# Kernel tuning notes

Measured on AMD Instinct MI355X. Metric: run time of the kernel, lower is better.

## Reference

```python
import jax, jax.numpy as jnp
import numpy as np

VOCAB = 32000
EMB = 256
HID = 512
SEQ = 512
SOS = 1  # word2vec key_to_index['<SOS>']; PAD assumed index 0 and never sampled


def setup_inputs() -> dict:
    key = jax.random.key(0)
    ks = jax.random.split(key, 8)
    k_lstm = 1.0 / np.sqrt(HID)
    k_out = 1.0 / np.sqrt(HID)
    return {
        # token ids in [2, VOCAB) so the PAD-skip branch never triggers
        "input_seq": jax.random.randint(ks[0], (1, SEQ), 2, VOCAB, dtype=jnp.int32),
        "h0": jnp.zeros((1, 1, HID), jnp.float32),
        "c0": jnp.zeros((1, 1, HID), jnp.float32),
        "embedding": jax.random.normal(ks[1], (VOCAB, EMB), jnp.float32) * 0.02,
        "W_ih": jax.random.uniform(ks[2], (4 * HID, EMB), jnp.float32, -k_lstm, k_lstm),
        "W_hh": jax.random.uniform(ks[3], (4 * HID, HID), jnp.float32, -k_lstm, k_lstm),
        "b_ih": jax.random.uniform(ks[4], (4 * HID,), jnp.float32, -k_lstm, k_lstm),
        "b_hh": jax.random.uniform(ks[5], (4 * HID,), jnp.float32, -k_lstm, k_lstm),
        "W_out": jax.random.uniform(ks[6], (VOCAB, HID), jnp.float32, -k_out, k_out),
        "b_out": jax.random.uniform(ks[7], (VOCAB,), jnp.float32, -k_out, k_out),
    }


def reference(input_seq, h0, c0, embedding, W_ih, W_hh, b_ih, b_hh, W_out, b_out):
    # tokens actually fed to the LSTM: <SOS> then the full teacher-forced sequence
    tokens = jnp.concatenate([jnp.array([SOS], jnp.int32), input_seq[0]])  # [S+1]
    emb = embedding[tokens]  # [S+1, E]
    bias = b_ih + b_hh

    def cell(carry, x_t):
        h, c = carry  # [H], [H]
        gates = W_ih @ x_t + W_hh @ h + bias  # [4H], torch gate order i,f,g,o
        i, f, g, o = jnp.split(gates, 4)
        i = jax.nn.sigmoid(i)
        f = jax.nn.sigmoid(f)
        g = jnp.tanh(g)
        o = jax.nn.sigmoid(o)
        c_new = f * c + i * g
        h_new = o * jnp.tanh(c_new)
        return (h_new, c_new), h_new

    (hT, cT), hs = jax.lax.scan(cell, (h0[0, 0], c0[0, 0]), emb)  # hs: [S+1, H]
    logits = hs @ W_out.T + b_out  # [S+1, V] (same math as per-step Linear + cat)
    outputs = logits[None]  # [1, S+1, V]
    return outputs, hT[None, None], cT[None, None]
```

## Files before the change

kernel.cpp:

```cpp
#include <hip/hip_runtime.h>
#include <cmath>

#define VOCAB 32000
#define EMB   256
#define HID   512
#define TLEN  513
#define G4    2048
#define NWG   32
#define SOS   1

typedef unsigned long long u64;
typedef unsigned int uivec4 __attribute__((ext_vector_type(4)));
typedef float f32x4 __attribute__((ext_vector_type(4)));
typedef short bf16x8 __attribute__((ext_vector_type(8)));

__device__ inline float fsig(float x)  { return __builtin_amdgcn_rcpf(1.f + __expf(-x)); }
__device__ inline float ftanh(float x) { return 1.f - 2.f * __builtin_amdgcn_rcpf(__expf(2.f * x) + 1.f); }

__device__ inline void bf16split(float f, short& h, short& l) {
    unsigned u = __float_as_uint(f);
    unsigned r = u + (0x7fffu + ((u >> 16) & 1u));
    unsigned hb = r & 0xffff0000u;
    h = (short)(hb >> 16);
    float res = f - __uint_as_float(hb);
    unsigned u2 = __float_as_uint(res);
    unsigned r2 = u2 + (0x7fffu + ((u2 >> 16) & 1u));
    l = (short)(r2 >> 16);
}

__global__ __launch_bounds__(256) void precompute_gates(
    const int* __restrict__ seq, const float* __restrict__ emb,
    const float* __restrict__ W_ih, const float* __restrict__ b_ih,
    const float* __restrict__ b_hh, float* __restrict__ Xg)
{
    __shared__ __align__(16) float ebuf[16][EMB];
    const int bt = blockIdx.x;
    const int br = blockIdx.y;
    const int tid = threadIdx.x;

    for (int tt = 0; tt < 16; ++tt) {
        int t = bt * 16 + tt;
        if (t < TLEN) {
            int tok = (t == 0) ? SOS : seq[t - 1];
            ebuf[tt][tid] = emb[(size_t)tok * EMB + tid];
        }
    }
    __syncthreads();

    const int row = br * 256 + tid;
    float acc[16];
#pragma unroll
    for (int tt = 0; tt < 16; ++tt) acc[tt] = 0.f;

    const float4* wp = (const float4*)(W_ih + (size_t)row * EMB);
#pragma unroll 4
    for (int k4 = 0; k4 < EMB / 4; ++k4) {
        float4 w = wp[k4];
#pragma unroll
        for (int tt = 0; tt < 16; ++tt) {
            float4 e = *(const float4*)&ebuf[tt][k4 * 4];
            acc[tt] = fmaf(w.x, e.x, fmaf(w.y, e.y, fmaf(w.z, e.z, fmaf(w.w, e.w, acc[tt]))));
        }
    }

    const float bias = b_ih[row] + b_hh[row];
    for (int tt = 0; tt < 16; ++tt) {
        int t = bt * 16 + tt;
        if (t < TLEN) Xg[(size_t)t * G4 + row] = acc[tt] + bias;
    }
}

__global__ __launch_bounds__(256, 1) void lstm_recurrence(
    const float* __restrict__ Xg, const float* __restrict__ W_hh,
    const float* __restrict__ h0, const float* __restrict__ c0,
    float* __restrict__ hs, u64* pk,
    float* __restrict__ out_hT, float* __restrict__ out_cT)
{
    __shared__ __align__(16) float hbuf[HID];
    __shared__ float pbuf[256];

    const int wg  = blockIdx.x;
    const int tid = threadIdx.x;
    const int wv  = tid >> 6;
    const int ln  = tid & 63;
    const int q   = ln >> 4;
    const int j   = ln & 15;
    const int row = q * HID + wg * 16 + j;

    float4 wreg[32];
    const float4* wp = (const float4*)(W_hh + (size_t)row * HID + wv * 128);
#pragma unroll
    for (int i = 0; i < 32; ++i) wreg[i] = wp[i];

    float c = (tid < 16) ? c0[wg * 16 + tid] : 0.f;
    {
        float2 h2 = *(const float2*)&h0[tid * 2];
        hbuf[tid * 2]     = h2.x;
        hbuf[tid * 2 + 1] = h2.y;
    }
    __syncthreads();

    for (int t = 0; t < TLEN; ++t) {
        float xg0 = 0.f, xg1 = 0.f, xg2 = 0.f, xg3 = 0.f;
        if (tid < 16) {
            const float* xp = Xg + (size_t)t * G4 + wg * 16 + tid;
            xg0 = xp[0]; xg1 = xp[512]; xg2 = xp[1024]; xg3 = xp[1536];
        }

        if (t > 0) {
            const unsigned tt = (unsigned)t;
            u64 sa = (u64)(uintptr_t)(pk + (size_t)(t & 1) * HID + 2 * tid);
            asm volatile("s_waitcnt vmcnt(0)" ::: "memory");
            uivec4 rA, rB;
            asm volatile("global_load_dwordx4 %0, %1, off sc0 sc1"
                         : "=v"(rA) : "v"(sa));
            asm volatile("global_load_dwordx4 %0, %1, off sc0 sc1\n\t"
                         "s_waitcnt vmcnt(1)"
                         : "=v"(rB) : "v"(sa));
            unsigned w0, w1;
            for (;;) {
                if (rA.y == tt && rA.w == tt) { w0 = rA.x; w1 = rA.z; break; }
                asm volatile("global_load_dwordx4 %0, %1, off sc0 sc1\n\t"
                             "s_waitcnt vmcnt(1)"
                             : "=v"(rA) : "v"(sa));
                if (rB.y == tt && rB.w == tt) { w0 = rB.x; w1 = rB.z; break; }
                asm volatile("global_load_dwordx4 %0, %1, off sc0 sc1\n\t"
                             "s_waitcnt vmcnt(1)"
                             : "=v"(rB) : "v"(sa));
            }
            asm volatile("s_waitcnt vmcnt(0)" : : "v"(rA), "v"(rB));
            hbuf[2 * tid]     = __uint_as_float(w0);
            hbuf[2 * tid + 1] = __uint_as_float(w1);
            __syncthreads();
        }

        float acc8[8];
#pragma unroll
        for (int i = 0; i < 8; ++i) acc8[i] = 0.f;
#pragma unroll
        for (int i = 0; i < 32; ++i) {
            float4 w4 = wreg[i];
            float4 h4 = *(const float4*)&hbuf[wv * 128 + i * 4];
            acc8[i & 7] = fmaf(w4.x, h4.x, fmaf(w4.y, h4.y,
                          fmaf(w4.z, h4.z, fmaf(w4.w, h4.w, acc8[i & 7]))));
        }
        pbuf[tid] = ((acc8[0] + acc8[1]) + (acc8[2] + acc8[3]))
                  + ((acc8[4] + acc8[5]) + (acc8[6] + acc8[7]));
        __syncthreads();

        if (tid < 16) {
            float gi = pbuf[tid]      + pbuf[64 + tid]  + pbuf[128 + tid] + pbuf[192 + tid] + xg0;
            float gf = pbuf[16 + tid] + pbuf[80 + tid]  + pbuf[144 + tid] + pbuf[208 + tid] + xg1;
            float gg = pbuf[32 + tid] + pbuf[96 + tid]  + pbuf[160 + tid] + pbuf[224 + tid] + xg2;
            float go = pbuf[48 + tid] + pbuf[112 + tid] + pbuf[176 + tid] + pbuf[240 + tid] + xg3;
            float i_ = fsig(gi);
            float f_ = fsig(gf);
            float g_ = ftanh(gg);
            float o_ = fsig(go);
            c = fmaf(f_, c, i_ * g_);
            float h_ = o_ * ftanh(c);
            if (t < TLEN - 1) {
                u64 word = ((u64)(unsigned)(t + 1) << 32) | (u64)__float_as_uint(h_);
                __hip_atomic_store(&pk[(size_t)((t + 1) & 1) * HID + wg * 16 + tid], word,
                                   __ATOMIC_RELAXED, __HIP_MEMORY_SCOPE_AGENT);
            } else {
                out_hT[wg * 16 + tid] = h_;
                out_cT[wg * 16 + tid] = c;
            }
            hs[(size_t)t * HID + wg * 16 + tid] = h_;
        }
    }
}

#define GLDT 40

__global__ __launch_bounds__(256, 2) void out_gemm_mfma(
    const float* __restrict__ hs, const float* __restrict__ W_out,
    const float* __restrict__ b_out, float* __restrict__ out)
{
    __shared__ __align__(16) short Ah[128][GLDT];
    __shared__ __align__(16) short Al[128][GLDT];
    __shared__ __align__(16) short Bh[128][GLDT];
    __shared__ __align__(16) short Bl[128][GLDT];

    const int tb = blockIdx.x;
    const int vb = blockIdx.y;
    const int tid = threadIdx.x;
    const int w   = tid >> 6;
    const int l   = tid & 63;
    const int l15 = l & 15;
    const int lg  = l >> 4;
    const int m0 = tb * 128, n0 = vb * 128;

    const int sr = tid >> 1;
    const int kh = (tid & 1) * 16;

    f32x4 acc[2][8];
#pragma unroll
    for (int s = 0; s < 2; ++s)
#pragma unroll
        for (int cc = 0; cc < 8; ++cc) acc[s][cc] = (f32x4){0.f, 0.f, 0.f, 0.f};

    for (int k0 = 0; k0 < HID; k0 += 32) {
        {
            int trow = m0 + sr;
            float4 fa0 = make_float4(0.f,0.f,0.f,0.f), fa1 = fa0, fa2 = fa0, fa3 = fa0;
            if (trow < TLEN) {
                const float4* ap = (const float4*)(hs + (size_t)trow * HID + k0 + kh);
                fa0 = ap[0]; fa1 = ap[1]; fa2 = ap[2]; fa3 = ap[3];
            }
            float fv[16] = { fa0.x,fa0.y,fa0.z,fa0.w, fa1.x,fa1.y,fa1.z,fa1.w,
                             fa2.x,fa2.y,fa2.z,fa2.w, fa3.x,fa3.y,fa3.z,fa3.w };
#pragma unroll
            for (int g = 0; g < 2; ++g) {
                union { short s[8]; bf16x8 v; } ph, pl;
#pragma unroll
                for (int e = 0; e < 8; ++e) bf16split(fv[g * 8 + e], ph.s[e], pl.s[e]);
                *(bf16x8*)&Ah[sr][kh + 8 * g] = ph.v;
                *(bf16x8*)&Al[sr][kh + 8 * g] = pl.v;
            }
        }
        {
            const float4* bp = (const float4*)(W_out + (size_t)(n0 + sr) * HID + k0 + kh);
            float4 fb0 = bp[0], fb1 = bp[1], fb2 = bp[2], fb3 = bp[3];
            float fv[16] = { fb0.x,fb0.y,fb0.z,fb0.w, fb1.x,fb1.y,fb1.z,fb1.w,
                             fb2.x,fb2.y,fb2.z,fb2.w, fb3.x,fb3.y,fb3.z,fb3.w };
#pragma unroll
            for (int g = 0; g < 2; ++g) {
                union { short s[8]; bf16x8 v; } ph, pl;
#pragma unroll
                for (int e = 0; e < 8; ++e) bf16split(fv[g * 8 + e], ph.s[e], pl.s[e]);
                *(bf16x8*)&Bh[sr][kh + 8 * g] = ph.v;
                *(bf16x8*)&Bl[sr][kh + 8 * g] = pl.v;
            }
        }
        __syncthreads();

        bf16x8 ah[2], al2[2];
#pragma unroll
        for (int s = 0; s < 2; ++s) {
            ah[s]  = *(const bf16x8*)&Ah[32 * w + 16 * s + l15][8 * lg];
            al2[s] = *(const bf16x8*)&Al[32 * w + 16 * s + l15][8 * lg];
        }
#pragma unroll
        for (int cc = 0; cc < 8; ++cc) {
            bf16x8 bh = *(const bf16x8*)&Bh[16 * cc + l15][8 * lg];
            bf16x8 bl = *(const bf16x8*)&Bl[16 * cc + l15][8 * lg];
#pragma unroll
            for (int s = 0; s < 2; ++s) {
                acc[s][cc] = __builtin_amdgcn_mfma_f32_16x16x32_bf16(ah[s],  bh, acc[s][cc], 0, 0, 0);
                acc[s][cc] = __builtin_amdgcn_mfma_f32_16x16x32_bf16(ah[s],  bl, acc[s][cc], 0, 0, 0);
                acc[s][cc] = __builtin_amdgcn_mfma_f32_16x16x32_bf16(al2[s], bh, acc[s][cc], 0, 0, 0);
            }
        }
        __syncthreads();
    }

#pragma unroll
    for (int cc = 0; cc < 8; ++cc) {
        int col = n0 + 16 * cc + l15;
        float bo = b_out[col];
#pragma unroll
        for (int s = 0; s < 2; ++s) {
            int rbase = m0 + 32 * w + 16 * s + lg * 4;
#pragma unroll
            for (int r = 0; r < 4; ++r) {
                int trow = rbase + r;
                if (trow < TLEN) out[(size_t)trow * VOCAB + col] = acc[s][cc][r] + bo;
            }
        }
    }
}

extern "C" void kernel_launch(void* const* d_in, const int* in_sizes, int n_in,
                              void* d_out, int out_size, void* d_ws, size_t ws_size,
                              hipStream_t stream)
{
    const int*   seq   = (const int*)  d_in[0];
    const float* h0    = (const float*)d_in[1];
    const float* c0    = (const float*)d_in[2];
    const float* emb   = (const float*)d_in[3];
    const float* W_ih  = (const float*)d_in[4];
    const float* W_hh  = (const float*)d_in[5];
    const float* b_ih  = (const float*)d_in[6];
    const float* b_hh  = (const float*)d_in[7];
    const float* W_out = (const float*)d_in[8];
    const float* b_out = (const float*)d_in[9];

    float* out_logits = (float*)d_out;
    float* out_hT     = out_logits + (size_t)TLEN * VOCAB;
    float* out_cT     = out_hT + HID;

    float* Xg = (float*)d_ws;
    float* hs = Xg + (size_t)TLEN * G4;
    u64*   pk = (u64*)(hs + (size_t)TLEN * HID);

    hipMemsetAsync(pk, 0, 2 * HID * sizeof(u64), stream);
    precompute_gates<<<dim3(33, 8), 256, 0, stream>>>(seq, emb, W_ih, b_ih, b_hh, Xg);
    lstm_recurrence<<<NWG, 256, 0, stream>>>(Xg, W_hh, h0, c0, hs, pk, out_hT, out_cT);
    out_gemm_mfma<<<dim3(5, 250), 256, 0, stream>>>(hs, W_out, b_out, out_logits);
}
```

Before: 1.073 ms.

## Add L2-local fast-path flag exchange with XCD-aware block placement in LSTM recurrence

The recurrence grid is launched with 249 blocks and only every eighth block does work. On a GPU that deals blocks round-robin across XCDs, this would put all 32 working blocks on the same XCD. Each step's h is published both to a system-coherent buffer and to a second buffer written and polled with sc0 only, so the poll can hit the shared L2 instead of going further out. The fast path has a bounded spin count and falls back to the coherent poll if any lane times out. The pbuf partial-sum buffer is double-buffered so the barrier after writing hbuf can be dropped. This relies on undocumented block-to-XCD placement, and the removed barrier may introduce races.

```diff
diff --git a/kernel.cpp b/kernel.cpp
--- a/kernel.cpp
+++ b/kernel.cpp
@@ -73,13 +73,15 @@
 __global__ __launch_bounds__(256, 1) void lstm_recurrence(
     const float* __restrict__ Xg, const float* __restrict__ W_hh,
     const float* __restrict__ h0, const float* __restrict__ c0,
-    float* __restrict__ hs, u64* pk,
+    float* __restrict__ hs, u64* pk, u64* pf,
     float* __restrict__ out_hT, float* __restrict__ out_cT)
 {
     __shared__ __align__(16) float hbuf[HID];
-    __shared__ float pbuf[256];
-
-    const int wg  = blockIdx.x;
+    __shared__ float pbuf[2][256];
+
+    const int bx = blockIdx.x;
+    if (bx & 7) return;
+    const int wg  = bx >> 3;
     const int tid = threadIdx.x;
     const int wv  = tid >> 6;
     const int ln  = tid & 63;
@@ -100,6 +102,8 @@
     }
     __syncthreads();
 
+    bool usefast = true;
+
     for (int t = 0; t < TLEN; ++t) {
         float xg0 = 0.f, xg1 = 0.f, xg2 = 0.f, xg3 = 0.f;
         if (tid < 16) {
@@ -109,29 +113,29 @@
 
         if (t > 0) {
             const unsigned tt = (unsigned)t;
-            u64 sa = (u64)(uintptr_t)(pk + (size_t)(t & 1) * HID + 2 * tid);
-            asm volatile("s_waitcnt vmcnt(0)" ::: "memory");
-            uivec4 rA, rB;
-            asm volatile("global_load_dwordx4 %0, %1, off sc0 sc1"
-                         : "=v"(rA) : "v"(sa));
-            asm volatile("global_load_dwordx4 %0, %1, off sc0 sc1\n\t"
-                         "s_waitcnt vmcnt(1)"
-                         : "=v"(rB) : "v"(sa));
-            unsigned w0, w1;
-            for (;;) {
-                if (rA.y == tt && rA.w == tt) { w0 = rA.x; w1 = rA.z; break; }
-                asm volatile("global_load_dwordx4 %0, %1, off sc0 sc1\n\t"
-                             "s_waitcnt vmcnt(1)"
-                             : "=v"(rA) : "v"(sa));
-                if (rB.y == tt && rB.w == tt) { w0 = rB.x; w1 = rB.z; break; }
-                asm volatile("global_load_dwordx4 %0, %1, off sc0 sc1\n\t"
-                             "s_waitcnt vmcnt(1)"
-                             : "=v"(rB) : "v"(sa));
-            }
-            asm volatile("s_waitcnt vmcnt(0)" : : "v"(rA), "v"(rB));
-            hbuf[2 * tid]     = __uint_as_float(w0);
-            hbuf[2 * tid + 1] = __uint_as_float(w1);
-            __syncthreads();
+            const size_t off = (size_t)(t & 1) * HID + 2 * tid;
+            uivec4 r;
+            bool got = false;
+            if (usefast) {
+                u64 fa = (u64)(uintptr_t)(pf + off);
+                const int K = (t == 1) ? 128 : 64;
+                for (int it = 0; it < K; ++it) {
+                    asm volatile("global_load_dwordx4 %0, %1, off sc0\n\t"
+                                 "s_waitcnt vmcnt(0)" : "=v"(r) : "v"(fa));
+                    if (r.y == tt && r.w == tt) { got = true; break; }
+                }
+                if (__ballot(got ? 1 : 0) != ~0ull) usefast = false;
+            }
+            if (!got) {
+                u64 sa = (u64)(uintptr_t)(pk + off);
+                do {
+                    asm volatile("global_load_dwordx4 %0, %1, off sc0 sc1\n\t"
+                                 "s_waitcnt vmcnt(0)" : "=v"(r) : "v"(sa));
+                } while (r.y != tt || r.w != tt);
+            }
+            hbuf[2 * tid]     = __uint_as_float(r.x);
+            hbuf[2 * tid + 1] = __uint_as_float(r.z);
+            asm volatile("s_waitcnt lgkmcnt(0)" ::: "memory");
         }
 
         float acc8[8];
@@ -144,15 +148,16 @@
             acc8[i & 7] = fmaf(w4.x, h4.x, fmaf(w4.y, h4.y,
                           fmaf(w4.z, h4.z, fmaf(w4.w, h4.w, acc8[i & 7]))));
         }
-        pbuf[tid] = ((acc8[0] + acc8[1]) + (acc8[2] + acc8[3]))
-                  + ((acc8[4] + acc8[5]) + (acc8[6] + acc8[7]));
+        pbuf[t & 1][tid] = ((acc8[0] + acc8[1]) + (acc8[2] + acc8[3]))
+                         + ((acc8[4] + acc8[5]) + (acc8[6] + acc8[7]));
         __syncthreads();
 
         if (tid < 16) {
-            float gi = pbuf[tid]      + pbuf[64 + tid]  + pbuf[128 + tid] + pbuf[192 + tid] + xg0;
-            float gf = pbuf[16 + tid] + pbuf[80 + tid]  + pbuf[144 + tid] + pbuf[208 + tid] + xg1;
-            float gg = pbuf[32 + tid] + pbuf[96 + tid]  + pbuf[160 + tid] + pbuf[224 + tid] + xg2;
-            float go = pbuf[48 + tid] + pbuf[112 + tid] + pbuf[176 + tid] + pbuf[240 + tid] + xg3;
+            const float* pb = pbuf[t & 1];
+            float gi = pb[tid]      + pb[64 + tid]  + pb[128 + tid] + pb[192 + tid] + xg0;
+            float gf = pb[16 + tid] + pb[80 + tid]  + pb[144 + tid] + pb[208 + tid] + xg1;
+            float gg = pb[32 + tid] + pb[96 + tid]  + pb[160 + tid] + pb[224 + tid] + xg2;
+            float go = pb[48 + tid] + pb[112 + tid] + pb[176 + tid] + pb[240 + tid] + xg3;
             float i_ = fsig(gi);
             float f_ = fsig(gf);
             float g_ = ftanh(gg);
@@ -161,8 +166,11 @@
             float h_ = o_ * ftanh(c);
             if (t < TLEN - 1) {
                 u64 word = ((u64)(unsigned)(t + 1) << 32) | (u64)__float_as_uint(h_);
-                __hip_atomic_store(&pk[(size_t)((t + 1) & 1) * HID + wg * 16 + tid], word,
-                                   __ATOMIC_RELAXED, __HIP_MEMORY_SCOPE_AGENT);
+                size_t po = (size_t)((t + 1) & 1) * HID + wg * 16 + tid;
+                u64 faddr = (u64)(uintptr_t)(pf + po);
+                asm volatile("global_store_dwordx2 %0, %1, off sc0"
+                             :: "v"(faddr), "v"(word) : "memory");
+                __hip_atomic_store(&pk[po], word, __ATOMIC_RELAXED, __HIP_MEMORY_SCOPE_AGENT);
             } else {
                 out_hT[wg * 16 + tid] = h_;
                 out_cT[wg * 16 + tid] = c;
@@ -294,9 +302,10 @@
     float* Xg = (float*)d_ws;
     float* hs = Xg + (size_t)TLEN * G4;
     u64*   pk = (u64*)(hs + (size_t)TLEN * HID);
-
-    hipMemsetAsync(pk, 0, 2 * HID * sizeof(u64), stream);
+    u64*   pf = pk + 2 * HID;
+
+    hipMemsetAsync(pk, 0, 4 * HID * sizeof(u64), stream);
     precompute_gates<<<dim3(33, 8), 256, 0, stream>>>(seq, emb, W_ih, b_ih, b_hh, Xg);
-    lstm_recurrence<<<NWG, 256, 0, stream>>>(Xg, W_hh, h0, c0, hs, pk, out_hT, out_cT);
+    lstm_recurrence<<<249, 256, 0, stream>>>(Xg, W_hh, h0, c0, hs, pk, pf, out_hT, out_cT);
     out_gemm_mfma<<<dim3(5, 250), 256, 0, stream>>>(hs, W_out, b_out, out_logits);
 }
```

Result: faster. 924.8 us (-13.8%).

## Restructure LSTM recurrence into 128 single-wave blocks with shuffle reductions

Applied to the files above, without the earlier changes.

The recurrence kernel moves from 32 workgroups of 256 threads to 128 single-wavefront blocks, each owning 4 hidden units. W_hh slices stay in registers, the previous h is read straight from the packed flag buffer into registers, and gate reductions use cross-lane shuffles instead of LDS and __syncthreads. The point is to remove intra-block barriers and LDS round trips from the serial per-step critical path. The cost is that 128 blocks now poll the global flag buffer each step. The separate memset of the flag buffer is also folded into the precompute kernel.

```diff
diff --git a/kernel.cpp b/kernel.cpp
--- a/kernel.cpp
+++ b/kernel.cpp
@@ -6,7 +6,7 @@
 #define HID   512
 #define TLEN  513
 #define G4    2048
-#define NWG   32
+#define NWAVE 128
 #define SOS   1
 
 typedef unsigned long long u64;
@@ -16,6 +16,9 @@
 
 __device__ inline float fsig(float x)  { return __builtin_amdgcn_rcpf(1.f + __expf(-x)); }
 __device__ inline float ftanh(float x) { return 1.f - 2.f * __builtin_amdgcn_rcpf(__expf(2.f * x) + 1.f); }
+__device__ inline float fma4(f32x4 w, f32x4 h, float a) {
+    return fmaf(w[0], h[0], fmaf(w[1], h[1], fmaf(w[2], h[2], fmaf(w[3], h[3], a))));
+}
 
 __device__ inline void bf16split(float f, short& h, short& l) {
     unsigned u = __float_as_uint(f);
@@ -31,13 +34,17 @@
 __global__ __launch_bounds__(256) void precompute_gates(
     const int* __restrict__ seq, const float* __restrict__ emb,
     const float* __restrict__ W_ih, const float* __restrict__ b_ih,
-    const float* __restrict__ b_hh, float* __restrict__ Xg)
+    const float* __restrict__ b_hh, float* __restrict__ Xg, u64* pk)
 {
     __shared__ __align__(16) float ebuf[16][EMB];
     const int bt = blockIdx.x;
     const int br = blockIdx.y;
     const int tid = threadIdx.x;
 
+    if (bt == 0 && br == 0) {
+        pk[tid] = 0; pk[tid + 256] = 0; pk[tid + 512] = 0; pk[tid + 768] = 0;
+    }
+
     for (int tt = 0; tt < 16; ++tt) {
         int t = bt * 16 + tt;
         if (t < TLEN) {
@@ -70,104 +77,118 @@
     }
 }
 
-__global__ __launch_bounds__(256, 1) void lstm_recurrence(
+__global__ __launch_bounds__(64, 1) void lstm_recurrence(
     const float* __restrict__ Xg, const float* __restrict__ W_hh,
     const float* __restrict__ h0, const float* __restrict__ c0,
     float* __restrict__ hs, u64* pk,
     float* __restrict__ out_hT, float* __restrict__ out_cT)
 {
-    __shared__ __align__(16) float hbuf[HID];
-    __shared__ float pbuf[256];
-
-    const int wg  = blockIdx.x;
-    const int tid = threadIdx.x;
-    const int wv  = tid >> 6;
-    const int ln  = tid & 63;
-    const int q   = ln >> 4;
-    const int j   = ln & 15;
-    const int row = q * HID + wg * 16 + j;
-
-    float4 wreg[32];
-    const float4* wp = (const float4*)(W_hh + (size_t)row * HID + wv * 128);
-#pragma unroll
-    for (int i = 0; i < 32; ++i) wreg[i] = wp[i];
-
-    float c = (tid < 16) ? c0[wg * 16 + tid] : 0.f;
+    const int W  = blockIdx.x;
+    const int ln = threadIdx.x;
+    const int qs = (ln >> 2) & 3;
+    const int ds = ln & 3;
+    const int j4 = 4 * W;
+
+    f32x4 wa[16], wb[16];
+#pragma unroll
+    for (int r = 0; r < 16; ++r) {
+        const float* wp = W_hh + ((size_t)(r >> 2) * HID + j4 + (r & 3)) * HID + 8 * ln;
+        wa[r] = *(const f32x4*)wp;
+        wb[r] = *(const f32x4*)(wp + 4);
+    }
+#pragma unroll
+    for (int r = 0; r < 16; ++r) {
+        asm volatile("" : "+v"(wa[r]), "+v"(wb[r]));
+    }
+
+    float c = (ln < 4) ? c0[j4 + ln] : 0.f;
+
+    f32x4 hA, hB;
     {
-        float2 h2 = *(const float2*)&h0[tid * 2];
-        hbuf[tid * 2]     = h2.x;
-        hbuf[tid * 2 + 1] = h2.y;
-    }
-    __syncthreads();
+        const float* hp = h0 + 8 * ln;
+        hA = *(const f32x4*)hp;
+        hB = *(const f32x4*)(hp + 4);
+    }
 
     for (int t = 0; t < TLEN; ++t) {
-        float xg0 = 0.f, xg1 = 0.f, xg2 = 0.f, xg3 = 0.f;
-        if (tid < 16) {
-            const float* xp = Xg + (size_t)t * G4 + wg * 16 + tid;
-            xg0 = xp[0]; xg1 = xp[512]; xg2 = xp[1024]; xg3 = xp[1536];
-        }
+        float xg = Xg[(size_t)t * G4 + qs * HID + j4 + ds];
 
         if (t > 0) {
             const unsigned tt = (unsigned)t;
-            u64 sa = (u64)(uintptr_t)(pk + (size_t)(t & 1) * HID + 2 * tid);
-            asm volatile("s_waitcnt vmcnt(0)" ::: "memory");
-            uivec4 rA, rB;
-            asm volatile("global_load_dwordx4 %0, %1, off sc0 sc1"
-                         : "=v"(rA) : "v"(sa));
-            asm volatile("global_load_dwordx4 %0, %1, off sc0 sc1\n\t"
-                         "s_waitcnt vmcnt(1)"
-                         : "=v"(rB) : "v"(sa));
-            unsigned w0, w1;
+            u64 sa = (u64)(uintptr_t)(pk + (size_t)(t & 1) * HID + 8 * ln);
+            uivec4 r0, r1, r2, r3;
             for (;;) {
-                if (rA.y == tt && rA.w == tt) { w0 = rA.x; w1 = rA.z; break; }
-                asm volatile("global_load_dwordx4 %0, %1, off sc0 sc1\n\t"
-                             "s_waitcnt vmcnt(1)"
-                             : "=v"(rA) : "v"(sa));
-                if (rB.y == tt && rB.w == tt) { w0 = rB.x; w1 = rB.z; break; }
-                asm volatile("global_load_dwordx4 %0, %1, off sc0 sc1\n\t"
-                             "s_waitcnt vmcnt(1)"
-                             : "=v"(rB) : "v"(sa));
-            }
-            asm volatile("s_waitcnt vmcnt(0)" : : "v"(rA), "v"(rB));
-            hbuf[2 * tid]     = __uint_as_float(w0);
-            hbuf[2 * tid + 1] = __uint_as_float(w1);
-            __syncthreads();
-        }
-
-        float acc8[8];
-#pragma unroll
-        for (int i = 0; i < 8; ++i) acc8[i] = 0.f;
-#pragma unroll
-        for (int i = 0; i < 32; ++i) {
-            float4 w4 = wreg[i];
-            float4 h4 = *(const float4*)&hbuf[wv * 128 + i * 4];
-            acc8[i & 7] = fmaf(w4.x, h4.x, fmaf(w4.y, h4.y,
-                          fmaf(w4.z, h4.z, fmaf(w4.w, h4.w, acc8[i & 7]))));
-        }
-        pbuf[tid] = ((acc8[0] + acc8[1]) + (acc8[2] + acc8[3]))
-                  + ((acc8[4] + acc8[5]) + (acc8[6] + acc8[7]));
-        __syncthreads();
-
-        if (tid < 16) {
-            float gi = pbuf[tid]      + pbuf[64 + tid]  + pbuf[128 + tid] + pbuf[192 + tid] + xg0;
-            float gf = pbuf[16 + tid] + pbuf[80 + tid]  + pbuf[144 + tid] + pbuf[208 + tid] + xg1;
-            float gg = pbuf[32 + tid] + pbuf[96 + tid]  + pbuf[160 + tid] + pbuf[224 + tid] + xg2;
-            float go = pbuf[48 + tid] + pbuf[112 + tid] + pbuf[176 + tid] + pbuf[240 + tid] + xg3;
-            float i_ = fsig(gi);
-            float f_ = fsig(gf);
-            float g_ = ftanh(gg);
-            float o_ = fsig(go);
-            c = fmaf(f_, c, i_ * g_);
-            float h_ = o_ * ftanh(c);
+                asm volatile(
+                    "global_load_dwordx4 %0, %4, off sc0 sc1\n\t"
+                    "global_load_dwordx4 %1, %4, off offset:16 sc0 sc1\n\t"
+                    "global_load_dwordx4 %2, %4, off offset:32 sc0 sc1\n\t"
+                    "global_load_dwordx4 %3, %4, off offset:48 sc0 sc1\n\t"
+                    "s_waitcnt vmcnt(0)"
+                    : "=&v"(r0), "=&v"(r1), "=&v"(r2), "=&v"(r3) : "v"(sa));
+                if (r0.y == tt && r0.w == tt && r1.y == tt && r1.w == tt &&
+                    r2.y == tt && r2.w == tt && r3.y == tt && r3.w == tt) break;
+            }
+            hA[0] = __uint_as_float(r0.x); hA[1] = __uint_as_float(r0.z);
+            hA[2] = __uint_as_float(r1.x); hA[3] = __uint_as_float(r1.z);
+            hB[0] = __uint_as_float(r2.x); hB[1] = __uint_as_float(r2.z);
+            hB[2] = __uint_as_float(r3.x); hB[3] = __uint_as_float(r3.z);
+        }
+
+        float p[16];
+#pragma unroll
+        for (int r = 0; r < 16; ++r)
+            p[r] = fma4(wa[r], hA, fma4(wb[r], hB, 0.f));
+
+        const bool b0 = (ln & 1), b1 = (ln & 2), b2 = (ln & 4), b3 = (ln & 8);
+        float q1[8];
+#pragma unroll
+        for (int i = 0; i < 8; ++i) {
+            float mine = b0 ? p[2*i+1] : p[2*i];
+            float send = b0 ? p[2*i]   : p[2*i+1];
+            q1[i] = mine + __shfl_xor(send, 1, 64);
+        }
+        float q2[4];
+#pragma unroll
+        for (int i = 0; i < 4; ++i) {
+            float mine = b1 ? q1[2*i+1] : q1[2*i];
+            float send = b1 ? q1[2*i]   : q1[2*i+1];
+            q2[i] = mine + __shfl_xor(send, 2, 64);
+        }
+        float q3[2];
+#pragma unroll
+        for (int i = 0; i < 2; ++i) {
+            float mine = b2 ? q2[2*i+1] : q2[2*i];
+            float send = b2 ? q2[2*i]   : q2[2*i+1];
+            q3[i] = mine + __shfl_xor(send, 4, 64);
+        }
+        float q4;
+        {
+            float mine = b3 ? q3[1] : q3[0];
+            float send = b3 ? q3[0] : q3[1];
+            q4 = mine + __shfl_xor(send, 8, 64);
+        }
+        q4 += __shfl_xor(q4, 16, 64);
+        q4 += __shfl_xor(q4, 32, 64);
+        float gate = q4 + xg;
+
+        float v = (qs == 2) ? ftanh(gate) : fsig(gate);
+        float iv = __shfl(v, ds,      64);
+        float fv = __shfl(v, 4 + ds,  64);
+        float gv = __shfl(v, 8 + ds,  64);
+        float ov = __shfl(v, 12 + ds, 64);
+        c = fmaf(fv, c, iv * gv);
+        float h_ = ov * ftanh(c);
+
+        if (ln < 4) {
             if (t < TLEN - 1) {
                 u64 word = ((u64)(unsigned)(t + 1) << 32) | (u64)__float_as_uint(h_);
-                __hip_atomic_store(&pk[(size_t)((t + 1) & 1) * HID + wg * 16 + tid], word,
+                __hip_atomic_store(&pk[(size_t)((t + 1) & 1) * HID + j4 + ln], word,
                                    __ATOMIC_RELAXED, __HIP_MEMORY_SCOPE_AGENT);
             } else {
-                out_hT[wg * 16 + tid] = h_;
-                out_cT[wg * 16 + tid] = c;
-            }
-            hs[(size_t)t * HID + wg * 16 + tid] = h_;
+                out_hT[j4 + ln] = h_;
+                out_cT[j4 + ln] = c;
+            }
+            hs[(size_t)t * HID + j4 + ln] = h_;
         }
     }
 }
@@ -295,8 +316,7 @@
     float* hs = Xg + (size_t)TLEN * G4;
     u64*   pk = (u64*)(hs + (size_t)TLEN * HID);
 
-    hipMemsetAsync(pk, 0, 2 * HID * sizeof(u64), stream);
-    precompute_gates<<<dim3(33, 8), 256, 0, stream>>>(seq, emb, W_ih, b_ih, b_hh, Xg);
-    lstm_recurrence<<<NWG, 256, 0, stream>>>(Xg, W_hh, h0, c0, hs, pk, out_hT, out_cT);
+    precompute_gates<<<dim3(33, 8), 256, 0, stream>>>(seq, emb, W_ih, b_ih, b_hh, Xg, pk);
+    lstm_recurrence<<<NWAVE, 64, 0, stream>>>(Xg, W_hh, h0, c0, hs, pk, out_hT, out_cT);
     out_gemm_mfma<<<dim3(5, 250), 256, 0, stream>>>(hs, W_out, b_out, out_logits);
 }
```

New measurement: 993.6 us. 1.08x faster.
